# Performance work log

Hardware: AMD Instinct MI355X
Metric: run time of the kernel (lower is better)

## Reference

```python
import jax, jax.numpy as jnp
import numpy as np

WEIGHT_SP = 0.1
BANDWIDTH = 0.5
EPS = 1e-5


def _l2_normalize(v, axis, eps=1e-12):
    # matches torch F.normalize(p=2): x / max(||x||, eps)
    n = jnp.sqrt(jnp.sum(v * v, axis=axis, keepdims=True))
    return v / jnp.maximum(n, eps)


def _compute_meshgrid(N, H, W):
    rows = jnp.arange(H, dtype=jnp.float32) / (H + 1)
    cols = jnp.arange(W, dtype=jnp.float32) / (W + 1)
    gr, gc = jnp.meshgrid(rows, cols, indexing="ij")
    grid = jnp.stack([gr, gc])[None]  # (1, 2, H, W)
    return jnp.broadcast_to(grid, (N, 2, H, W))


def _l2_distance(x, y):
    # Faithful to the torch code; its broadcasting is only valid for N == 1.
    N, C, H, W = x.shape
    xv = x.reshape(N, C, -1)
    yv = y.reshape(N, C, -1)
    x_s = jnp.sum(xv ** 2, axis=1)          # (N, HW)
    y_s = jnp.sum(yv ** 2, axis=1)          # (N, HW)
    A = jnp.einsum("nci,ncj->nij", yv, xv)  # (N, HW, HW)
    dist = y_s - 2.0 * A + x_s.T            # same broadcast as torch (N==1)
    dist = jnp.swapaxes(dist, 1, 2)         # transpose(1,2); reshape is no-op
    return jnp.maximum(dist, 0.0)


def _cosine_distance(x, y):
    y_mu = jnp.mean(y, axis=(0, 2, 3), keepdims=True)   # (1, C, 1, 1)
    xn = _l2_normalize(x - y_mu, axis=1)
    yn = _l2_normalize(y - y_mu, axis=1)
    N, C = x.shape[:2]
    xn = xn.reshape(N, C, -1)
    yn = yn.reshape(N, C, -1)
    cos = jnp.einsum("nci,ncj->nij", xn, yn)            # (N, HW, HW)
    return 1.0 - cos


def _relative_distance(dist, eps=1e-5):
    dmin = jnp.min(dist, axis=2, keepdims=True)
    return dist / (dmin + eps)


def _compute_cx(dist_tilde, bandwidth):
    w = jnp.exp((1.0 - dist_tilde) / bandwidth)
    return w / jnp.sum(w, axis=2, keepdims=True)


def setup_inputs() -> dict:
    key = jax.random.key(0)
    k1, k2 = jax.random.split(key)
    x = jax.random.normal(k1, (1, 512, 80, 80), dtype=jnp.float32)
    y = jax.random.normal(k2, (1, 512, 80, 80), dtype=jnp.float32)
    return {"x": x, "y": y}


def reference(x, y):
    N, C, H, W = x.shape
    # spatial branch
    grid = _compute_meshgrid(N, H, W)
    cx_sp = _compute_cx(_relative_distance(_l2_distance(grid, grid), 1e-5), BANDWIDTH)
    # feature branch (loss_type == 'cosine')
    cx_feat = _compute_cx(_relative_distance(_cosine_distance(x, y), EPS), BANDWIDTH)
    cx_combine = (1.0 - WEIGHT_SP) * cx_feat + WEIGHT_SP * cx_sp
    k_max = jnp.max(cx_combine, axis=2, keepdims=True)  # (N, HW, 1)
    cx = jnp.mean(k_max, axis=1)                        # (N, 1)
    return jnp.mean(-jnp.log(cx + EPS))
```

## Files before the change

### kernel.cpp

```cpp
#include <hip/hip_runtime.h>
#include <hip/hip_bf16.h>
#include <math.h>

#define HW 6400
#define NC 512
#define NH 80
#define NW 80
#define NCH 25
#define NSLOT 50
#define NCYS 8
#define JCH 256
#define TI 128
#define BK 64
#define NT16 400

typedef __attribute__((ext_vector_type(8))) short short8;
typedef __attribute__((ext_vector_type(4))) float v4f;

#define MU_OFF    0
#define INVD_OFF  512
#define GMAXP_OFF (512 + HW)
#define ZP_OFF    (GMAXP_OFF + HW*NSLOT)
#define WDP_OFF   (ZP_OFF + HW*NSLOT)
#define ACC_OFF   (WDP_OFF + HW*NCYS)
#define F32_FLOATS (ACC_OFF + 64)
#define XB_BYTE   ((size_t)(((F32_FLOATS*4) + 255) & ~255))
#define YB_BYTE   (XB_BYTE + (size_t)HW*NC*2)
#define G_BYTE    (YB_BYTE + (size_t)HW*NC*2)
#define G_BYTES   ((size_t)NT16 * NT16 * 256 * 2)

typedef __attribute__((address_space(1))) unsigned int uint_g;
typedef __attribute__((address_space(3))) unsigned int uint_l;
__device__ __forceinline__ void gload16(const void* g, void* l) {
    __builtin_amdgcn_global_load_lds((const uint_g*)g, (uint_l*)l, 16, 0, 0);
}

__global__ void k_mu(const float* __restrict__ y, float* __restrict__ mu) {
    int c = blockIdx.x;
    const float* yc = y + (size_t)c * HW;
    float s = 0.f;
    for (int i = threadIdx.x; i < HW; i += 256) s += yc[i];
    __shared__ float red[256];
    red[threadIdx.x] = s;
    __syncthreads();
    for (int off = 128; off > 0; off >>= 1) {
        if (threadIdx.x < off) red[threadIdx.x] += red[threadIdx.x + off];
        __syncthreads();
    }
    if (threadIdx.x == 0) mu[c] = red[0] * (1.0f / HW);
}

__global__ void k_sumsq(const float* __restrict__ x, const float* __restrict__ y,
                        const float* __restrict__ mu,
                        float* __restrict__ psx, float* __restrict__ psy) {
    int i = blockIdx.x * 256 + threadIdx.x;
    int c0 = blockIdx.y * 64;
    float sx = 0.f, sy = 0.f;
    for (int c = c0; c < c0 + 64; ++c) {
        float m = mu[c];
        float dx = x[(size_t)c * HW + i] - m;
        float dy = y[(size_t)c * HW + i] - m;
        sx = fmaf(dx, dx, sx);
        sy = fmaf(dy, dy, sy);
    }
    psx[(size_t)blockIdx.y * HW + i] = sx;
    psy[(size_t)blockIdx.y * HW + i] = sy;
}

__global__ void k_transpose(const float* __restrict__ x, const float* __restrict__ y,
                            const float* __restrict__ mu,
                            const float* __restrict__ psx, const float* __restrict__ psy,
                            unsigned short* __restrict__ xb, unsigned short* __restrict__ yb) {
    __shared__ float tile[64 * 68];
    __shared__ float ssinv[64];
    const int t = threadIdx.x;
    const int i0 = blockIdx.x * 64;
    const int c0 = blockIdx.y * 64;
    const int z = blockIdx.z;
    const float* src = z ? y : x;
    const float* ps  = z ? psy : psx;
    unsigned short* dst = z ? yb : xb;

    if (t < 64) {
        float s = 0.f;
        #pragma unroll
        for (int p = 0; p < 8; ++p) s += ps[(size_t)p * HW + i0 + t];
        ssinv[t] = 1.0f / fmaxf(sqrtf(s), 1e-12f);
    }
    __syncthreads();
    #pragma unroll 4
    for (int it = 0; it < 16; ++it) {
        int cl = it * 4 + (t >> 6);
        int il = t & 63;
        float v = (src[(size_t)(c0 + cl) * HW + i0 + il] - mu[c0 + cl]) * ssinv[il];
        tile[il * 68 + cl] = v;
    }
    __syncthreads();
    #pragma unroll
    for (int it = 0; it < 2; ++it) {
        int il = t >> 2;
        int seg = (t & 3) + it * 4;
        unsigned int pk[4];
        #pragma unroll
        for (int p = 0; p < 4; ++p) {
            float v0 = tile[il * 68 + seg * 8 + p * 2];
            float v1 = tile[il * 68 + seg * 8 + p * 2 + 1];
            __hip_bfloat16 h0 = __float2bfloat16(v0);
            __hip_bfloat16 h1 = __float2bfloat16(v1);
            unsigned short u0 = *reinterpret_cast<unsigned short*>(&h0);
            unsigned short u1 = *reinterpret_cast<unsigned short*>(&h1);
            pk[p] = (unsigned int)u0 | ((unsigned int)u1 << 16);
        }
        uint4 val = make_uint4(pk[0], pk[1], pk[2], pk[3]);
        *(uint4*)&dst[(size_t)(i0 + il) * NC + c0 + seg * 8] = val;
    }
}

template <typename F>
__device__ __forceinline__ void gemm_driver(const unsigned short* __restrict__ Xb,
                                            const unsigned short* __restrict__ Yb,
                                            F&& consume) {
    __shared__ char sA[TI * BK * 2];
    __shared__ char sB[TI * BK * 2];
    const int t = threadIdx.x;
    const int w = t >> 6, l = t & 63;
    const int wr = w >> 1, wc = w & 1;
    const int lr = l & 15, lg = l >> 4;
    const int i0 = blockIdx.x * TI;
    const int jbase = blockIdx.y * JCH;

    int aoff[4][2], boff[4][2];
    #pragma unroll
    for (int mt = 0; mt < 4; ++mt) {
        int row = wr * 64 + mt * 16 + lr;
        #pragma unroll
        for (int ks = 0; ks < 2; ++ks) {
            int seg = ks * 4 + lg;
            aoff[mt][ks] = row * 128 + ((seg ^ (row & 7)) * 16);
        }
    }
    #pragma unroll
    for (int nt = 0; nt < 4; ++nt) {
        int row = wc * 64 + nt * 16 + lr;
        #pragma unroll
        for (int ks = 0; ks < 2; ++ks) {
            int seg = ks * 4 + lg;
            boff[nt][ks] = row * 128 + ((seg ^ (row & 7)) * 16);
        }
    }

    const int strow = l >> 3;
    const int stcol = ((l & 7) ^ strow) * 8;
    char* dA0 = sA + (w * 4 + 0) * 1024;
    char* dA1 = sA + (w * 4 + 1) * 1024;
    char* dA2 = sA + (w * 4 + 2) * 1024;
    char* dA3 = sA + (w * 4 + 3) * 1024;
    char* dB0 = sB + (w * 4 + 0) * 1024;
    char* dB1 = sB + (w * 4 + 1) * 1024;
    char* dB2 = sB + (w * 4 + 2) * 1024;
    char* dB3 = sB + (w * 4 + 3) * 1024;
    const unsigned short* ga = Xb + (size_t)(i0 + w * 32 + strow) * NC + stcol;
    const unsigned short* gb0 = Yb + (size_t)(jbase + w * 32 + strow) * NC + stcol;

    #pragma unroll 1
    for (int jt = 0; jt < JCH; jt += TI) {
        const unsigned short* gb = gb0 + (size_t)jt * NC;
        v4f acc[4][4];
        #pragma unroll
        for (int mt = 0; mt < 4; ++mt)
            #pragma unroll
            for (int nt = 0; nt < 4; ++nt)
                acc[mt][nt] = (v4f){0.f, 0.f, 0.f, 0.f};

        #pragma unroll 1
        for (int kt = 0; kt < NC; kt += BK) {
            __syncthreads();
            gload16(ga + kt,           dA0);
            gload16(ga + 8  * NC + kt, dA1);
            gload16(ga + 16 * NC + kt, dA2);
            gload16(ga + 24 * NC + kt, dA3);
            gload16(gb + kt,           dB0);
            gload16(gb + 8  * NC + kt, dB1);
            gload16(gb + 16 * NC + kt, dB2);
            gload16(gb + 24 * NC + kt, dB3);
            __syncthreads();
            #pragma unroll
            for (int ks = 0; ks < 2; ++ks) {
                short8 af[4], bf[4];
                #pragma unroll
                for (int mt = 0; mt < 4; ++mt) af[mt] = *(const short8*)&sA[aoff[mt][ks]];
                #pragma unroll
                for (int nt = 0; nt < 4; ++nt) bf[nt] = *(const short8*)&sB[boff[nt][ks]];
                #pragma unroll
                for (int mt = 0; mt < 4; ++mt)
                    #pragma unroll
                    for (int nt = 0; nt < 4; ++nt)
                        acc[mt][nt] = __builtin_amdgcn_mfma_f32_16x16x32_bf16(
                            af[mt], bf[nt], acc[mt][nt], 0, 0, 0);
            }
        }
        consume(acc, jt);
    }
}

__device__ __forceinline__ void rmax_epilogue(float (&rmax)[16], float* gmaxp,
                                              int i0, int wr, int wc, int lr, int lg) {
    #pragma unroll
    for (int u = 0; u < 16; ++u) {
        float v = rmax[u];
        v = fmaxf(v, __shfl_xor(v, 1));
        v = fmaxf(v, __shfl_xor(v, 2));
        v = fmaxf(v, __shfl_xor(v, 4));
        v = fmaxf(v, __shfl_xor(v, 8));
        if (lr == 0) {
            int row = i0 + wr * 64 + (u >> 2) * 16 + lg * 4 + (u & 3);
            gmaxp[(size_t)row * NSLOT + blockIdx.y * 2 + wc] = v;
        }
    }
}

__global__ __launch_bounds__(256, 2) void k_pass1s(const unsigned short* __restrict__ Xb,
                                                   const unsigned short* __restrict__ Yb,
                                                   float* __restrict__ gmaxp,
                                                   unsigned int* __restrict__ G2) {
    const int t = threadIdx.x;
    const int w = t >> 6, l = t & 63;
    const int wr = w >> 1, wc = w & 1;
    const int lr = l & 15, lg = l >> 4;
    const int i0 = blockIdx.x * TI;
    const int jbase = blockIdx.y * JCH;
    float rmax[16];
    #pragma unroll
    for (int u = 0; u < 16; ++u) rmax[u] = -3.0e38f;

    gemm_driver(Xb, Yb, [&](v4f (&acc)[4][4], int jt) {
        #pragma unroll
        for (int mt = 0; mt < 4; ++mt) {
            size_t rbase = (size_t)(i0 / 16 + wr * 4 + mt) * (NT16 * 128);
            #pragma unroll
            for (int nt = 0; nt < 4; ++nt) {
                int ct = (jbase + jt) / 16 + wc * 4 + nt;
                unsigned int pk0, pk1;
                {
                    __hip_bfloat16 h0 = __float2bfloat16(acc[mt][nt][0]);
                    __hip_bfloat16 h1 = __float2bfloat16(acc[mt][nt][1]);
                    __hip_bfloat16 h2 = __float2bfloat16(acc[mt][nt][2]);
                    __hip_bfloat16 h3 = __float2bfloat16(acc[mt][nt][3]);
                    pk0 = (unsigned int)*(unsigned short*)&h0 | ((unsigned int)*(unsigned short*)&h1 << 16);
                    pk1 = (unsigned int)*(unsigned short*)&h2 | ((unsigned int)*(unsigned short*)&h3 << 16);
                }
                *(uint2*)&G2[(rbase + (size_t)ct * 128 + l * 2)] = make_uint2(pk0, pk1);
                #pragma unroll
                for (int r = 0; r < 4; ++r)
                    rmax[mt * 4 + r] = fmaxf(rmax[mt * 4 + r], acc[mt][nt][r]);
            }
        }
    });
    rmax_epilogue(rmax, gmaxp, i0, wr, wc, lr, lg);
}

__global__ __launch_bounds__(256) void k_pass2s(const unsigned int* __restrict__ G2,
                                                const float* __restrict__ gmaxp,
                                                float* __restrict__ zp,
                                                float* __restrict__ wdp) {
    const int t = threadIdx.x;
    const int w = t >> 6, l = t & 63;
    const int lr = l & 15, lg = l >> 4;
    const int rt = blockIdx.x * 4 + w;
    const int cy = blockIdx.y;

    float m = -3.0e38f;
    {
        int row = rt * 16 + lr;
        #pragma unroll
        for (int k = 0; k < 13; ++k) {
            int s = lg + 4 * k;
            if (s < NSLOT) m = fmaxf(m, gmaxp[(size_t)row * NSLOT + s]);
        }
        m = fmaxf(m, __shfl_xor(m, 16));
        m = fmaxf(m, __shfl_xor(m, 32));
    }
    float inv_lr = 1.0f / ((1.0f - m) + 1e-5f);
    float c1[4], c2[4];
    #pragma unroll
    for (int r = 0; r < 4; ++r) {
        float iv = __shfl(inv_lr, lg * 4 + r);
        c2[r] = 2.0f * iv;
        c1[r] = 2.0f - 2.0f * iv;
    }

    const uint2* base = (const uint2*)G2 + (size_t)rt * (NT16 * 64) + l;
    float zs[4] = {0.f, 0.f, 0.f, 0.f};
    #pragma unroll 4
    for (int ct = cy * 50; ct < cy * 50 + 50; ++ct) {
        uint2 v = base[(size_t)ct * 64];
        float g0 = __uint_as_float((v.x & 0xFFFFu) << 16);
        float g1 = __uint_as_float(v.x & 0xFFFF0000u);
        float g2 = __uint_as_float((v.y & 0xFFFFu) << 16);
        float g3 = __uint_as_float(v.y & 0xFFFF0000u);
        zs[0] += __expf(fmaf(c2[0], g0, c1[0]));
        zs[1] += __expf(fmaf(c2[1], g1, c1[1]));
        zs[2] += __expf(fmaf(c2[2], g2, c1[2]));
        zs[3] += __expf(fmaf(c2[3], g3, c1[3]));
    }
    float wd[4] = {0.f, 0.f, 0.f, 0.f};
    if (rt / 50 == cy) {
        uint2 v = base[(size_t)rt * 64];
        float g[4];
        g[0] = __uint_as_float((v.x & 0xFFFFu) << 16);
        g[1] = __uint_as_float(v.x & 0xFFFF0000u);
        g[2] = __uint_as_float((v.y & 0xFFFFu) << 16);
        g[3] = __uint_as_float(v.y & 0xFFFF0000u);
        #pragma unroll
        for (int r = 0; r < 4; ++r)
            if (lr == lg * 4 + r) wd[r] = __expf(fmaf(c2[r], g[r], c1[r]));
    }
    #pragma unroll
    for (int r = 0; r < 4; ++r) {
        float z = zs[r], d = wd[r];
        z += __shfl_xor(z, 1);  d += __shfl_xor(d, 1);
        z += __shfl_xor(z, 2);  d += __shfl_xor(d, 2);
        z += __shfl_xor(z, 4);  d += __shfl_xor(d, 4);
        z += __shfl_xor(z, 8);  d += __shfl_xor(d, 8);
        if (lr == 0) {
            int row = rt * 16 + lg * 4 + r;
            zp[(size_t)row * NCYS + cy] = z;
            wdp[(size_t)row * NCYS + cy] = d;
        }
    }
}

__global__ void k_kmax_s(const float* __restrict__ zp, const float* __restrict__ wdp,
                         const float* __restrict__ gmaxp, float* __restrict__ accum,
                         int* __restrict__ counter, float* __restrict__ out) {
    int i = blockIdx.x * 256 + threadIdx.x;
    float Z = 0.f, wd = 0.f, gmax = -3.0e38f;
    #pragma unroll
    for (int s = 0; s < NCYS; ++s) {
        Z += zp[(size_t)i * NCYS + s];
        wd += wdp[(size_t)i * NCYS + s];
    }
    #pragma unroll
    for (int s = 0; s < NSLOT; ++s) gmax = fmaxf(gmax, gmaxp[(size_t)i * NSLOT + s]);
    float dmin = 1.0f - gmax;
    float inv = 1.0f / (dmin + 1e-5f);
    float wmx = __expf(2.0f - 2.0f * dmin * inv);
    float invZ = 1.0f / Z;
    float kmax = fmaxf(0.9f * wmx * invZ, 0.9f * wd * invZ + 0.1f);

    __shared__ float red[256];
    red[threadIdx.x] = kmax;
    __syncthreads();
    for (int off = 128; off > 0; off >>= 1) {
        if (threadIdx.x < off) red[threadIdx.x] += red[threadIdx.x + off];
        __syncthreads();
    }
    if (threadIdx.x == 0) {
        atomicAdd(accum, red[0]);
        __threadfence();
        int n = atomicAdd(counter, 1);
        if (n == (int)gridDim.x - 1) {
            float total = atomicAdd(accum, 0.0f);
            out[0] = -logf(total * (1.0f / HW) + 1e-5f);
        }
    }
}

__global__ __launch_bounds__(256, 2) void k_pass1(const unsigned short* __restrict__ Xb,
                                                  const unsigned short* __restrict__ Yb,
                                                  float* __restrict__ gmaxp) {
    const int t = threadIdx.x;
    const int w = t >> 6, l = t & 63;
    const int wr = w >> 1, wc = w & 1;
    const int lr = l & 15, lg = l >> 4;
    const int i0 = blockIdx.x * TI;
    float rmax[16];
    #pragma unroll
    for (int u = 0; u < 16; ++u) rmax[u] = -3.0e38f;
    gemm_driver(Xb, Yb, [&](v4f (&acc)[4][4], int jt) {
        (void)jt;
        #pragma unroll
        for (int mt = 0; mt < 4; ++mt)
            #pragma unroll
            for (int r = 0; r < 4; ++r) {
                float mm = acc[mt][0][r];
                #pragma unroll
                for (int nt = 1; nt < 4; ++nt) mm = fmaxf(mm, acc[mt][nt][r]);
                rmax[mt * 4 + r] = fmaxf(rmax[mt * 4 + r], mm);
            }
    });
    rmax_epilogue(rmax, gmaxp, i0, wr, wc, lr, lg);
}

__global__ void k_invd(const float* __restrict__ gmaxp, float* __restrict__ invd) {
    int i = blockIdx.x * 256 + threadIdx.x;
    float m = -3.0e38f;
    #pragma unroll
    for (int s = 0; s < NSLOT; ++s) m = fmaxf(m, gmaxp[(size_t)i * NSLOT + s]);
    invd[i] = 1.0f / ((1.0f - m) + 1e-5f);
}

__global__ __launch_bounds__(256, 2) void k_pass2(const unsigned short* __restrict__ Xb,
                                                  const unsigned short* __restrict__ Yb,
                                                  const float* __restrict__ invd,
                                                  float* __restrict__ zp) {
    const int t = threadIdx.x;
    const int w = t >> 6, l = t & 63;
    const int wr = w >> 1, wc = w & 1;
    const int lr = l & 15, lg = l >> 4;
    const int i0 = blockIdx.x * TI;
    float zs[16], c1[16], c2[16];
    #pragma unroll
    for (int u = 0; u < 16; ++u) {
        int row = i0 + wr * 64 + (u >> 2) * 16 + lg * 4 + (u & 3);
        float inv = invd[row];
        c2[u] = 2.0f * inv;
        c1[u] = 2.0f - 2.0f * inv;
        zs[u] = 0.f;
    }
    gemm_driver(Xb, Yb, [&](v4f (&acc)[4][4], int jt) {
        (void)jt;
        #pragma unroll
        for (int mt = 0; mt < 4; ++mt)
            #pragma unroll
            for (int r = 0; r < 4; ++r) {
                int u = mt * 4 + r;
                float s = 0.f;
                #pragma unroll
                for (int nt = 0; nt < 4; ++nt)
                    s += __expf(fmaf(c2[u], acc[mt][nt][r], c1[u]));
                zs[u] += s;
            }
    });
    #pragma unroll
    for (int u = 0; u < 16; ++u) {
        float z = zs[u];
        z += __shfl_xor(z, 1);
        z += __shfl_xor(z, 2);
        z += __shfl_xor(z, 4);
        z += __shfl_xor(z, 8);
        if (lr == 0) {
            int row = i0 + wr * 64 + (u >> 2) * 16 + lg * 4 + (u & 3);
            zp[(size_t)row * NSLOT + blockIdx.y * 2 + wc] = z;
        }
    }
}

__global__ void k_kmax(const float* __restrict__ zp, const float* __restrict__ gmaxp,
                       const unsigned short* __restrict__ Xb, const unsigned short* __restrict__ Yb,
                       float* __restrict__ accum, int* __restrict__ counter,
                       float* __restrict__ out) {
    int i = blockIdx.x * 256 + threadIdx.x;
    float Z = 0.f, gmax = -3.0e38f;
    #pragma unroll
    for (int s = 0; s < NSLOT; ++s) {
        Z += zp[(size_t)i * NSLOT + s];
        gmax = fmaxf(gmax, gmaxp[(size_t)i * NSLOT + s]);
    }
    float gii = 0.f;
    const uint2* xr = (const uint2*)(Xb + (size_t)i * NC);
    const uint2* yr = (const uint2*)(Yb + (size_t)i * NC);
    for (int c4 = 0; c4 < NC / 4; ++c4) {
        uint2 xa = xr[c4], ya = yr[c4];
        float x0 = __uint_as_float((xa.x & 0xFFFFu) << 16), y0 = __uint_as_float((ya.x & 0xFFFFu) << 16);
        float x1 = __uint_as_float(xa.x & 0xFFFF0000u),     y1 = __uint_as_float(ya.x & 0xFFFF0000u);
        float x2 = __uint_as_float((xa.y & 0xFFFFu) << 16), y2 = __uint_as_float((ya.y & 0xFFFFu) << 16);
        float x3 = __uint_as_float(xa.y & 0xFFFF0000u),     y3 = __uint_as_float(ya.y & 0xFFFF0000u);
        gii = fmaf(x0, y0, gii); gii = fmaf(x1, y1, gii);
        gii = fmaf(x2, y2, gii); gii = fmaf(x3, y3, gii);
    }
    float dmin = 1.0f - gmax;
    float inv = 1.0f / (dmin + 1e-5f);
    float wmx = __expf(2.0f - 2.0f * dmin * inv);
    float wii = __expf(2.0f - 2.0f * (1.0f - gii) * inv);
    float invZ = 1.0f / Z;
    float kmax = fmaxf(0.9f * wmx * invZ, 0.9f * wii * invZ + 0.1f);

    __shared__ float red[256];
    red[threadIdx.x] = kmax;
    __syncthreads();
    for (int off = 128; off > 0; off >>= 1) {
        if (threadIdx.x < off) red[threadIdx.x] += red[threadIdx.x + off];
        __syncthreads();
    }
    if (threadIdx.x == 0) {
        atomicAdd(accum, red[0]);
        __threadfence();
        int n = atomicAdd(counter, 1);
        if (n == (int)gridDim.x - 1) {
            float total = atomicAdd(accum, 0.0f);
            out[0] = -logf(total * (1.0f / HW) + 1e-5f);
        }
    }
}

extern "C" void kernel_launch(void* const* d_in, const int* in_sizes, int n_in,
                              void* d_out, int out_size, void* d_ws, size_t ws_size,
                              hipStream_t stream) {
    const float* x = (const float*)d_in[0];
    const float* y = (const float*)d_in[1];
    float* out = (float*)d_out;
    float* ws = (float*)d_ws;

    float* mu    = ws + MU_OFF;
    float* invd  = ws + INVD_OFF;
    float* gmaxp = ws + GMAXP_OFF;
    float* psx   = ws + GMAXP_OFF;
    float* psy   = ws + GMAXP_OFF + 8 * HW;
    float* zp    = ws + ZP_OFF;
    float* wdp   = ws + WDP_OFF;
    float* accum = ws + ACC_OFF;
    int*   counter = (int*)(accum + 1);
    unsigned short* Xb = (unsigned short*)((char*)d_ws + XB_BYTE);
    unsigned short* Yb = (unsigned short*)((char*)d_ws + YB_BYTE);
    unsigned int*   G2 = (unsigned int*)((char*)d_ws + G_BYTE);

    const bool bigws = ws_size >= (G_BYTE + G_BYTES);

    hipMemsetAsync(accum, 0, 8, stream);

    hipLaunchKernelGGL(k_mu, dim3(NC), dim3(256), 0, stream, y, mu);
    hipLaunchKernelGGL(k_sumsq, dim3(HW / 256, NC / 64), dim3(256), 0, stream, x, y, mu, psx, psy);
    hipLaunchKernelGGL(k_transpose, dim3(HW / 64, NC / 64, 2), dim3(256), 0, stream,
                       x, y, mu, psx, psy, Xb, Yb);

    dim3 grid(HW / TI, NCH);
    if (bigws) {
        hipLaunchKernelGGL(k_pass1s, grid, dim3(256), 0, stream, Xb, Yb, gmaxp, G2);
        hipLaunchKernelGGL(k_pass2s, dim3(NT16 / 4, NCYS), dim3(256), 0, stream, G2, gmaxp, zp, wdp);
        hipLaunchKernelGGL(k_kmax_s, dim3(HW / 256), dim3(256), 0, stream, zp, wdp, gmaxp,
                           accum, counter, out);
    } else {
        hipLaunchKernelGGL(k_pass1, grid, dim3(256), 0, stream, Xb, Yb, gmaxp);
        hipLaunchKernelGGL(k_invd, dim3(HW / 256), dim3(256), 0, stream, gmaxp, invd);
        hipLaunchKernelGGL(k_pass2, grid, dim3(256), 0, stream, Xb, Yb, invd, zp);
        hipLaunchKernelGGL(k_kmax, dim3(HW / 256), dim3(256), 0, stream, zp, gmaxp, Xb, Yb,
                           accum, counter, out);
    }
}
```

Measured before the change: 166.2 us.

## Store intermediate similarity matrix in FP8 and capture diagonal in pass one

The stored cosine-similarity matrix between the two passes is now packed as FP8 instead of BF16, which halves the bytes written in pass one and read back in pass two. The diagonal entries are written at full precision from pass one, so pass two no longer computes the self-weight term. The mean and transpose kernels also switch to float4 loads, with the transpose tile stride changed from 68 to 65. FP8 quantisation of the similarities adds error to the exponentiated softmax denominator and may affect accuracy.

```diff
diff --git a/kernel.cpp b/kernel.cpp
--- a/kernel.cpp
+++ b/kernel.cpp
@@ -18,16 +18,15 @@
 typedef __attribute__((ext_vector_type(4))) float v4f;
 
 #define MU_OFF    0
-#define INVD_OFF  512
-#define GMAXP_OFF (512 + HW)
-#define ZP_OFF    (GMAXP_OFF + HW*NSLOT)
-#define WDP_OFF   (ZP_OFF + HW*NSLOT)
-#define ACC_OFF   (WDP_OFF + HW*NCYS)
-#define F32_FLOATS (ACC_OFF + 64)
+#define ACC_OFF   512
+#define GMAXP_OFF (ACC_OFF + 64)
+#define GDIAG_OFF (GMAXP_OFF + HW*NSLOT)
+#define ZP_OFF    (GDIAG_OFF + HW)
+#define F32_FLOATS (ZP_OFF + HW*NSLOT)
 #define XB_BYTE   ((size_t)(((F32_FLOATS*4) + 255) & ~255))
 #define YB_BYTE   (XB_BYTE + (size_t)HW*NC*2)
 #define G_BYTE    (YB_BYTE + (size_t)HW*NC*2)
-#define G_BYTES   ((size_t)NT16 * NT16 * 256 * 2)
+#define G_BYTES   ((size_t)NT16 * NT16 * 256)
 
 typedef __attribute__((address_space(1))) unsigned int uint_g;
 typedef __attribute__((address_space(3))) unsigned int uint_l;
@@ -37,9 +36,12 @@
 
 __global__ void k_mu(const float* __restrict__ y, float* __restrict__ mu) {
     int c = blockIdx.x;
-    const float* yc = y + (size_t)c * HW;
+    const float4* yc4 = (const float4*)(y + (size_t)c * HW);
     float s = 0.f;
-    for (int i = threadIdx.x; i < HW; i += 256) s += yc[i];
+    for (int i = threadIdx.x; i < HW / 4; i += 256) {
+        float4 v = yc4[i];
+        s += (v.x + v.y) + (v.z + v.w);
+    }
     __shared__ float red[256];
     red[threadIdx.x] = s;
     __syncthreads();
@@ -71,7 +73,7 @@
                             const float* __restrict__ mu,
                             const float* __restrict__ psx, const float* __restrict__ psy,
                             unsigned short* __restrict__ xb, unsigned short* __restrict__ yb) {
-    __shared__ float tile[64 * 68];
+    __shared__ float tile[64 * 65];
     __shared__ float ssinv[64];
     const int t = threadIdx.x;
     const int i0 = blockIdx.x * 64;
@@ -88,12 +90,16 @@
         ssinv[t] = 1.0f / fmaxf(sqrtf(s), 1e-12f);
     }
     __syncthreads();
-    #pragma unroll 4
-    for (int it = 0; it < 16; ++it) {
-        int cl = it * 4 + (t >> 6);
-        int il = t & 63;
-        float v = (src[(size_t)(c0 + cl) * HW + i0 + il] - mu[c0 + cl]) * ssinv[il];
-        tile[il * 68 + cl] = v;
+    #pragma unroll
+    for (int it = 0; it < 4; ++it) {
+        int cl = it * 16 + (t >> 4);
+        int p0 = (t & 15) * 4;
+        float4 v = *(const float4*)(src + (size_t)(c0 + cl) * HW + i0 + p0);
+        float m = mu[c0 + cl];
+        tile[(p0 + 0) * 65 + cl] = (v.x - m) * ssinv[p0 + 0];
+        tile[(p0 + 1) * 65 + cl] = (v.y - m) * ssinv[p0 + 1];
+        tile[(p0 + 2) * 65 + cl] = (v.z - m) * ssinv[p0 + 2];
+        tile[(p0 + 3) * 65 + cl] = (v.w - m) * ssinv[p0 + 3];
     }
     __syncthreads();
     #pragma unroll
@@ -103,8 +109,8 @@
         unsigned int pk[4];
         #pragma unroll
         for (int p = 0; p < 4; ++p) {
-            float v0 = tile[il * 68 + seg * 8 + p * 2];
-            float v1 = tile[il * 68 + seg * 8 + p * 2 + 1];
+            float v0 = tile[il * 65 + seg * 8 + p * 2];
+            float v1 = tile[il * 65 + seg * 8 + p * 2 + 1];
             __hip_bfloat16 h0 = __float2bfloat16(v0);
             __hip_bfloat16 h1 = __float2bfloat16(v1);
             unsigned short u0 = *reinterpret_cast<unsigned short*>(&h0);
@@ -113,6 +119,22 @@
         }
         uint4 val = make_uint4(pk[0], pk[1], pk[2], pk[3]);
         *(uint4*)&dst[(size_t)(i0 + il) * NC + c0 + seg * 8] = val;
+    }
+}
+
+__device__ __forceinline__ void rmax_epilogue(float (&rmax)[16], float* gmaxp,
+                                              int i0, int wr, int wc, int lr, int lg) {
+    #pragma unroll
+    for (int u = 0; u < 16; ++u) {
+        float v = rmax[u];
+        v = fmaxf(v, __shfl_xor(v, 1));
+        v = fmaxf(v, __shfl_xor(v, 2));
+        v = fmaxf(v, __shfl_xor(v, 4));
+        v = fmaxf(v, __shfl_xor(v, 8));
+        if (lr == 0) {
+            int row = i0 + wr * 64 + (u >> 2) * 16 + lg * 4 + (u & 3);
+            gmaxp[(size_t)row * NSLOT + blockIdx.y * 2 + wc] = v;
+        }
     }
 }
 
@@ -148,7 +170,6 @@
             boff[nt][ks] = row * 128 + ((seg ^ (row & 7)) * 16);
         }
     }
-
     const int strow = l >> 3;
     const int stcol = ((l & 7) ^ strow) * 8;
     char* dA0 = sA + (w * 4 + 0) * 1024;
@@ -203,26 +224,11 @@
     }
 }
 
-__device__ __forceinline__ void rmax_epilogue(float (&rmax)[16], float* gmaxp,
-                                              int i0, int wr, int wc, int lr, int lg) {
-    #pragma unroll
-    for (int u = 0; u < 16; ++u) {
-        float v = rmax[u];
-        v = fmaxf(v, __shfl_xor(v, 1));
-        v = fmaxf(v, __shfl_xor(v, 2));
-        v = fmaxf(v, __shfl_xor(v, 4));
-        v = fmaxf(v, __shfl_xor(v, 8));
-        if (lr == 0) {
-            int row = i0 + wr * 64 + (u >> 2) * 16 + lg * 4 + (u & 3);
-            gmaxp[(size_t)row * NSLOT + blockIdx.y * 2 + wc] = v;
-        }
-    }
-}
-
 __global__ __launch_bounds__(256, 2) void k_pass1s(const unsigned short* __restrict__ Xb,
                                                    const unsigned short* __restrict__ Yb,
                                                    float* __restrict__ gmaxp,
-                                                   unsigned int* __restrict__ G2) {
+                                                   float* __restrict__ gdiag,
+                                                   unsigned int* __restrict__ G1) {
     const int t = threadIdx.x;
     const int w = t >> 6, l = t & 63;
     const int wr = w >> 1, wc = w & 1;
@@ -234,35 +240,41 @@
     for (int u = 0; u < 16; ++u) rmax[u] = -3.0e38f;
 
     gemm_driver(Xb, Yb, [&](v4f (&acc)[4][4], int jt) {
+        const bool diagblk = (jbase + jt == i0);
         #pragma unroll
         for (int mt = 0; mt < 4; ++mt) {
-            size_t rbase = (size_t)(i0 / 16 + wr * 4 + mt) * (NT16 * 128);
+            size_t rbase = (size_t)(i0 / 16 + wr * 4 + mt) * (NT16 * 64);
             #pragma unroll
             for (int nt = 0; nt < 4; ++nt) {
                 int ct = (jbase + jt) / 16 + wc * 4 + nt;
-                unsigned int pk0, pk1;
-                {
-                    __hip_bfloat16 h0 = __float2bfloat16(acc[mt][nt][0]);
-                    __hip_bfloat16 h1 = __float2bfloat16(acc[mt][nt][1]);
-                    __hip_bfloat16 h2 = __float2bfloat16(acc[mt][nt][2]);
-                    __hip_bfloat16 h3 = __float2bfloat16(acc[mt][nt][3]);
-                    pk0 = (unsigned int)*(unsigned short*)&h0 | ((unsigned int)*(unsigned short*)&h1 << 16);
-                    pk1 = (unsigned int)*(unsigned short*)&h2 | ((unsigned int)*(unsigned short*)&h3 << 16);
+                float g0 = acc[mt][nt][0];
+                float g1 = acc[mt][nt][1];
+                float g2 = acc[mt][nt][2];
+                float g3 = acc[mt][nt][3];
+                rmax[mt * 4 + 0] = fmaxf(rmax[mt * 4 + 0], g0);
+                rmax[mt * 4 + 1] = fmaxf(rmax[mt * 4 + 1], g1);
+                rmax[mt * 4 + 2] = fmaxf(rmax[mt * 4 + 2], g2);
+                rmax[mt * 4 + 3] = fmaxf(rmax[mt * 4 + 3], g3);
+                unsigned int pk = __builtin_amdgcn_cvt_pk_fp8_f32(g0, g1, 0, false);
+                pk = __builtin_amdgcn_cvt_pk_fp8_f32(g2, g3, pk, true);
+                G1[rbase + (size_t)ct * 64 + l] = pk;
+                if (diagblk) {
+                    int rowb = i0 + wr * 64 + mt * 16 + lg * 4;
+                    int col = jbase + jt + wc * 64 + nt * 16 + lr;
+                    if (col == rowb + 0) gdiag[col] = g0;
+                    if (col == rowb + 1) gdiag[col] = g1;
+                    if (col == rowb + 2) gdiag[col] = g2;
+                    if (col == rowb + 3) gdiag[col] = g3;
                 }
-                *(uint2*)&G2[(rbase + (size_t)ct * 128 + l * 2)] = make_uint2(pk0, pk1);
-                #pragma unroll
-                for (int r = 0; r < 4; ++r)
-                    rmax[mt * 4 + r] = fmaxf(rmax[mt * 4 + r], acc[mt][nt][r]);
             }
         }
     });
     rmax_epilogue(rmax, gmaxp, i0, wr, wc, lr, lg);
 }
 
-__global__ __launch_bounds__(256) void k_pass2s(const unsigned int* __restrict__ G2,
+__global__ __launch_bounds__(256) void k_pass2s(const unsigned int* __restrict__ G1,
                                                 const float* __restrict__ gmaxp,
-                                                float* __restrict__ zp,
-                                                float* __restrict__ wdp) {
+                                                float* __restrict__ zp) {
     const int t = threadIdx.x;
     const int w = t >> 6, l = t & 63;
     const int lr = l & 15, lg = l >> 4;
@@ -289,64 +301,49 @@
         c1[r] = 2.0f - 2.0f * iv;
     }
 
-    const uint2* base = (const uint2*)G2 + (size_t)rt * (NT16 * 64) + l;
+    const unsigned int* base = G1 + (size_t)rt * (NT16 * 64) + l;
     float zs[4] = {0.f, 0.f, 0.f, 0.f};
     #pragma unroll 4
     for (int ct = cy * 50; ct < cy * 50 + 50; ++ct) {
-        uint2 v = base[(size_t)ct * 64];
-        float g0 = __uint_as_float((v.x & 0xFFFFu) << 16);
-        float g1 = __uint_as_float(v.x & 0xFFFF0000u);
-        float g2 = __uint_as_float((v.y & 0xFFFFu) << 16);
-        float g3 = __uint_as_float(v.y & 0xFFFF0000u);
+        unsigned int v = base[(size_t)ct * 64];
+        float g0 = __builtin_amdgcn_cvt_f32_fp8(v, 0);
+        float g1 = __builtin_amdgcn_cvt_f32_fp8(v, 1);
+        float g2 = __builtin_amdgcn_cvt_f32_fp8(v, 2);
+        float g3 = __builtin_amdgcn_cvt_f32_fp8(v, 3);
         zs[0] += __expf(fmaf(c2[0], g0, c1[0]));
         zs[1] += __expf(fmaf(c2[1], g1, c1[1]));
         zs[2] += __expf(fmaf(c2[2], g2, c1[2]));
         zs[3] += __expf(fmaf(c2[3], g3, c1[3]));
     }
-    float wd[4] = {0.f, 0.f, 0.f, 0.f};
-    if (rt / 50 == cy) {
-        uint2 v = base[(size_t)rt * 64];
-        float g[4];
-        g[0] = __uint_as_float((v.x & 0xFFFFu) << 16);
-        g[1] = __uint_as_float(v.x & 0xFFFF0000u);
-        g[2] = __uint_as_float((v.y & 0xFFFFu) << 16);
-        g[3] = __uint_as_float(v.y & 0xFFFF0000u);
-        #pragma unroll
-        for (int r = 0; r < 4; ++r)
-            if (lr == lg * 4 + r) wd[r] = __expf(fmaf(c2[r], g[r], c1[r]));
-    }
     #pragma unroll
     for (int r = 0; r < 4; ++r) {
-        float z = zs[r], d = wd[r];
-        z += __shfl_xor(z, 1);  d += __shfl_xor(d, 1);
-        z += __shfl_xor(z, 2);  d += __shfl_xor(d, 2);
-        z += __shfl_xor(z, 4);  d += __shfl_xor(d, 4);
-        z += __shfl_xor(z, 8);  d += __shfl_xor(d, 8);
+        float z = zs[r];
+        z += __shfl_xor(z, 1);
+        z += __shfl_xor(z, 2);
+        z += __shfl_xor(z, 4);
+        z += __shfl_xor(z, 8);
         if (lr == 0) {
             int row = rt * 16 + lg * 4 + r;
             zp[(size_t)row * NCYS + cy] = z;
-            wdp[(size_t)row * NCYS + cy] = d;
-        }
-    }
-}
-
-__global__ void k_kmax_s(const float* __restrict__ zp, const float* __restrict__ wdp,
+        }
+    }
+}
+
+__global__ void k_kmax_s(const float* __restrict__ zp, const float* __restrict__ gdiag,
                          const float* __restrict__ gmaxp, float* __restrict__ accum,
                          int* __restrict__ counter, float* __restrict__ out) {
     int i = blockIdx.x * 256 + threadIdx.x;
-    float Z = 0.f, wd = 0.f, gmax = -3.0e38f;
-    #pragma unroll
-    for (int s = 0; s < NCYS; ++s) {
-        Z += zp[(size_t)i * NCYS + s];
-        wd += wdp[(size_t)i * NCYS + s];
-    }
+    float Z = 0.f, gmax = -3.0e38f;
+    #pragma unroll
+    for (int s = 0; s < NCYS; ++s) Z += zp[(size_t)i * NCYS + s];
     #pragma unroll
     for (int s = 0; s < NSLOT; ++s) gmax = fmaxf(gmax, gmaxp[(size_t)i * NSLOT + s]);
     float dmin = 1.0f - gmax;
     float inv = 1.0f / (dmin + 1e-5f);
     float wmx = __expf(2.0f - 2.0f * dmin * inv);
+    float wii = __expf(2.0f - 2.0f * (1.0f - gdiag[i]) * inv);
     float invZ = 1.0f / Z;
-    float kmax = fmaxf(0.9f * wmx * invZ, 0.9f * wd * invZ + 0.1f);
+    float kmax = fmaxf(0.9f * wmx * invZ, 0.9f * wii * invZ + 0.1f);
 
     __shared__ float red[256];
     red[threadIdx.x] = kmax;
@@ -503,21 +500,20 @@
     float* ws = (float*)d_ws;
 
     float* mu    = ws + MU_OFF;
-    float* invd  = ws + INVD_OFF;
+    float* accum = ws + ACC_OFF;
+    int*   counter = (int*)(accum + 1);
     float* gmaxp = ws + GMAXP_OFF;
     float* psx   = ws + GMAXP_OFF;
     float* psy   = ws + GMAXP_OFF + 8 * HW;
+    float* gdiag = ws + GDIAG_OFF;
     float* zp    = ws + ZP_OFF;
-    float* wdp   = ws + WDP_OFF;
-    float* accum = ws + ACC_OFF;
-    int*   counter = (int*)(accum + 1);
     unsigned short* Xb = (unsigned short*)((char*)d_ws + XB_BYTE);
     unsigned short* Yb = (unsigned short*)((char*)d_ws + YB_BYTE);
-    unsigned int*   G2 = (unsigned int*)((char*)d_ws + G_BYTE);
+    unsigned int*   G1 = (unsigned int*)((char*)d_ws + G_BYTE);
 
     const bool bigws = ws_size >= (G_BYTE + G_BYTES);
 
-    hipMemsetAsync(accum, 0, 8, stream);
+    hipMemsetAsync(accum, 0, 64 * sizeof(float), stream);
 
     hipLaunchKernelGGL(k_mu, dim3(NC), dim3(256), 0, stream, y, mu);
     hipLaunchKernelGGL(k_sumsq, dim3(HW / 256, NC / 64), dim3(256), 0, stream, x, y, mu, psx, psy);
@@ -526,14 +522,14 @@
 
     dim3 grid(HW / TI, NCH);
     if (bigws) {
-        hipLaunchKernelGGL(k_pass1s, grid, dim3(256), 0, stream, Xb, Yb, gmaxp, G2);
-        hipLaunchKernelGGL(k_pass2s, dim3(NT16 / 4, NCYS), dim3(256), 0, stream, G2, gmaxp, zp, wdp);
-        hipLaunchKernelGGL(k_kmax_s, dim3(HW / 256), dim3(256), 0, stream, zp, wdp, gmaxp,
+        hipLaunchKernelGGL(k_pass1s, grid, dim3(256), 0, stream, Xb, Yb, gmaxp, gdiag, G1);
+        hipLaunchKernelGGL(k_pass2s, dim3(NT16 / 4, NCYS), dim3(256), 0, stream, G1, gmaxp, zp);
+        hipLaunchKernelGGL(k_kmax_s, dim3(HW / 256), dim3(256), 0, stream, zp, gdiag, gmaxp,
                            accum, counter, out);
     } else {
         hipLaunchKernelGGL(k_pass1, grid, dim3(256), 0, stream, Xb, Yb, gmaxp);
-        hipLaunchKernelGGL(k_invd, dim3(HW / 256), dim3(256), 0, stream, gmaxp, invd);
-        hipLaunchKernelGGL(k_pass2, grid, dim3(256), 0, stream, Xb, Yb, invd, zp);
+        hipLaunchKernelGGL(k_invd, dim3(HW / 256), dim3(256), 0, stream, gmaxp, gdiag);
+        hipLaunchKernelGGL(k_pass2, grid, dim3(256), 0, stream, Xb, Yb, gdiag, zp);
         hipLaunchKernelGGL(k_kmax, dim3(HW / 256), dim3(256), 0, stream, zp, gmaxp, Xb, Yb,
                            accum, counter, out);
     }
```

After: 156.2 us. -6.0%, faster.
